# Performance work log

Hardware: AMD Instinct MI355X
Metric: run time of the kernel (lower is better)

The kernel has to match this reference:

```python
import jax, jax.numpy as jnp
import numpy as np

B, N, F_IN, F_HID, F_EMB, H, L_DIM = 8, 1024, 128, 128, 128, 8, 2


def _xavier(key, shape, fan_in, fan_out):
    lim = np.sqrt(6.0 / (fan_in + fan_out))
    return jax.random.uniform(key, shape, jnp.float32, -lim, lim)


def setup_inputs() -> dict:
    key = jax.random.key(0)
    ks = jax.random.split(key, 16)
    x = jax.random.normal(ks[0], (B, N, F_IN), jnp.float32)
    # sparse 0/1 adjacency with self loops (avoids fully-masked softmax rows)
    adj = (jax.random.uniform(ks[1], (B, N, N)) < 0.05).astype(jnp.float32)
    adj = jnp.maximum(adj, jnp.eye(N, dtype=jnp.float32)[None])
    def gat_params(k, f_in, f_out):
        k1, k2, k3 = jax.random.split(k, 3)
        return (_xavier(k1, (H, f_in, f_out), f_in, f_out),
                _xavier(k2, (H, f_out, 1), f_out, 1),
                _xavier(k3, (H, f_out, 1), f_out, 1),
                jnp.zeros((f_out,), jnp.float32))
    w1, as1, ad1, b1 = gat_params(ks[2], F_IN, F_HID)
    w2, as2, ad2, b2 = gat_params(ks[3], F_HID, F_HID)
    w3, as3, ad3, b3 = gat_params(ks[4], F_HID, F_EMB)
    pred_in = F_HID * 2 + F_EMB  # hidden*(num_layers-1)+embedding, concat=True
    pw = _xavier(ks[5], (pred_in, L_DIM), pred_in, L_DIM)
    pb = jnp.zeros((L_DIM,), jnp.float32)
    return {"x": x, "adj": adj,
            "w1": w1, "as1": as1, "ad1": ad1, "b1": b1,
            "w2": w2, "as2": as2, "ad2": ad2, "b2": b2,
            "w3": w3, "as3": as3, "ad3": ad3, "b3": b3,
            "pw": pw, "pb": pb}


def gat_layer(h, adj, w, a_src, a_dst, bias):
    # h: [B,N,f_in] -> h_prime: [B,H,N,f_out]
    hp = jnp.einsum('bnf,hfo->bhno', h, w)
    t = jnp.tanh(hp)
    s = jnp.einsum('bhno,hoi->bhni', t, a_src)[..., 0]  # [B,H,N]
    d = jnp.einsum('bhno,hoi->bhni', t, a_dst)[..., 0]  # [B,H,N]
    scores = s[:, :, :, None] + d[:, :, None, :]        # [B,H,N,N]
    scores = jnp.where(scores >= 0, scores, 0.2 * scores)  # LeakyReLU(0.2)
    scores = jnp.where(adj[:, None, :, :] > 0, scores, -jnp.inf)
    attn = jax.nn.softmax(scores, axis=-1)  # dropout disabled (eval mode)
    out = jnp.einsum('bhnm,bhmo->bhno', attn, hp) + bias
    return out.mean(axis=1)  # merge heads -> [B,N,f_out]


def reference(x, adj, w1, as1, ad1, b1, w2, as2, ad2, b2, w3, as3, ad3, b3, pw, pb):
    x1 = jax.nn.relu(gat_layer(x, adj, w1, as1, ad1, b1))
    x2 = jax.nn.relu(gat_layer(x1, adj, w2, as2, ad2, b2))
    x3 = gat_layer(x2, adj, w3, as3, ad3, b3)
    x_all = jnp.concatenate([x1, x2, x3], axis=2)  # [B,N,pred_in]
    pooled = jnp.max(x_all, axis=1)                # max over nodes -> [B,pred_in]
    return pooled @ pw + pb                        # [B,label_dim]
```

## Files before the change

kernel.cpp:

```cpp
#include <hip/hip_runtime.h>
#include <hip/hip_fp16.h>

#define BB 8
#define NN 1024
#define FF 128
#define HH 8

typedef _Float16 f16;
typedef f16  f16x8 __attribute__((ext_vector_type(8)));
typedef f16  f16x4 __attribute__((ext_vector_type(4)));
typedef float f32x4 __attribute__((ext_vector_type(4)));

#define L2E 1.44269504f

__global__ void k_pre(const float* __restrict__ x, f16* __restrict__ x16a,
                      const float* __restrict__ w1, const float* __restrict__ w2,
                      const float* __restrict__ w3, f16* __restrict__ wB,
                      const float* __restrict__ adj, unsigned* __restrict__ am){
  int bid = blockIdx.x, t = threadIdx.x;
  if (bid < 512){
    int i = (bid*256 + t)*8;
    float4 a = *(const float4*)(x+i), b = *(const float4*)(x+i+4);
    f16x8 v;
    v[0]=(f16)a.x; v[1]=(f16)a.y; v[2]=(f16)a.z; v[3]=(f16)a.w;
    v[4]=(f16)b.x; v[5]=(f16)b.y; v[6]=(f16)b.z; v[7]=(f16)b.w;
    *(f16x8*)(x16a+i) = v;
  } else if (bid < 704){
    int e = (bid-512)*256 + t;
    int fc = e & 15, c = (e>>4)&127, h = (e>>11)&7, l = e>>14;
    const float* w = (l==0) ? w1 : ((l==1) ? w2 : w3);
    f16x8 v;
    #pragma unroll
    for(int j=0;j<8;j++) v[j] = (f16)w[(h*128 + fc*8 + j)*128 + c];
    *(f16x8*)(wB + (((l*8+h)*16 + fc)*128 + c)*8) = v;
  } else {
    int wv = t >> 6, lane = t & 63;
    int r = (bid-704)*4 + wv;
    const float* row = adj + (long)r*1024;
    for(int g=0; g<16; g++){
      float v = row[g*64 + lane];
      unsigned long long mb = __ballot(v > 0.0f);
      if (lane == 0){
        am[r*32 + 2*g]   = (unsigned)mb;
        am[r*32 + 2*g+1] = (unsigned)(mb >> 32);
      }
    }
  }
}

__global__ __launch_bounds__(256,2) void k_hp(
    const f16* __restrict__ xin,
    const f16* __restrict__ wBl,
    const float* __restrict__ asrc, const float* __restrict__ adst,
    f16* __restrict__ hpB,
    float* __restrict__ sarr, float* __restrict__ darr)
{
  __shared__ f16 xs[128*136];
  __shared__ float asl[128], adl[128];
  int t = threadIdx.x;
  int bid = blockIdx.x;
  int it = bid & 7, h = (bid>>3)&7, b = bid>>6;
  int i0 = it*128;
  {
    const f16* src = xin + (long)(b*1024 + i0)*128;
    int fc = t & 15, r0 = t >> 4;
    #pragma unroll
    for(int p=0;p<8;p++){
      int r = r0 + p*16;
      f16x8 v = *(const f16x8*)(src + r*128 + fc*8);
      *(f16x8*)(xs + r*136 + fc*8) = v;
    }
  }
  if (t < 128){ asl[t] = asrc[h*128+t]; adl[t] = adst[h*128+t]; }
  __syncthreads();

  int lane = t & 63, wv = t>>6, wr = wv>>1, wc = wv&1;
  int mq = lane & 15, quad = lane >> 4;
  f32x4 acc[4][4];
  #pragma unroll
  for(int a=0;a<4;a++)
    #pragma unroll
    for(int c=0;c<4;c++) acc[a][c] = (f32x4){0.f,0.f,0.f,0.f};

  const f16* wh = wBl + h*16*128*8;
  #pragma unroll
  for(int ks=0; ks<4; ks++){
    f16x8 af[4], bf[4];
    #pragma unroll
    for(int mt=0; mt<4; mt++)
      af[mt] = *(const f16x8*)(xs + (wr*64 + mt*16 + mq)*136 + ks*32 + quad*8);
    #pragma unroll
    for(int nt=0; nt<4; nt++){
      int c  = wc*64 + nt*16 + mq;
      int fc = ks*4 + quad;
      bf[nt] = *(const f16x8*)(wh + (fc*128 + c)*8);
    }
    #pragma unroll
    for(int mt=0; mt<4; mt++)
      #pragma unroll
      for(int nt=0; nt<4; nt++)
        acc[mt][nt] = __builtin_amdgcn_mfma_f32_16x16x32_f16(af[mt], bf[nt], acc[mt][nt], 0,0,0);
  }
  __syncthreads();
  f16* tt = xs;
  f16* hpb = hpB + (long)(b*8+h)*128*128*8;
  #pragma unroll
  for(int mt=0; mt<4; mt++){
    #pragma unroll
    for(int nt=0; nt<4; nt++){
      int c = wc*64 + nt*16 + mq;
      f16x4 pk;
      #pragma unroll
      for(int rg=0; rg<4; rg++){
        float v = acc[mt][nt][rg];
        pk[rg] = (f16)v;
        int il = wr*64 + mt*16 + quad*4 + rg;
        float e2 = __expf(2.0f*v);
        float th = 1.0f - 2.0f*__builtin_amdgcn_rcpf(e2 + 1.0f);
        tt[il*136 + c] = (f16)th;
      }
      int il0 = wr*64 + mt*16 + quad*4;
      int inode = i0 + il0;
      *(f16x4*)(hpb + ((long)(inode>>3)*128 + c)*8 + (inode&7)) = pk;
    }
  }
  __syncthreads();
  {
    int r = t>>1, hf = t&1;
    float s_p = 0.f, d_p = 0.f;
    #pragma unroll
    for(int q=0;q<8;q++){
      f16x8 tv = *(const f16x8*)(tt + r*136 + hf*64 + q*8);
      #pragma unroll
      for(int j=0;j<8;j++){
        float tvf = (float)tv[j];
        int c = hf*64 + q*8 + j;
        s_p = fmaf(tvf, asl[c], s_p);
        d_p = fmaf(tvf, adl[c], d_p);
      }
    }
    s_p += __shfl_xor(s_p, 1);
    d_p += __shfl_xor(d_p, 1);
    if (hf == 0){
      sarr[(b*8+h)*1024 + i0 + r] = s_p;
      darr[(b*8+h)*1024 + i0 + r] = d_p;
    }
  }
}

__global__ __launch_bounds__(256,4) void k_attn(
    const f16* __restrict__ hpB,
    const float* __restrict__ sarr, const float* __restrict__ darr,
    const unsigned* __restrict__ am,
    f16* __restrict__ part,
    float* __restrict__ zpart)
{
  __shared__ float ddl[512];
  __shared__ float wred[4];
  __shared__ f16 Pl[2][128*40];
  int t = threadIdx.x;
  int bid = blockIdx.x;
  int bh = bid & 63, q = bid >> 6;
  int jh = q & 1, it = q >> 1;
  int i0 = it*128, j0 = jh*512;
  int b = bh >> 3;

  {
    float4 v = *(const float4*)(darr + bh*1024 + t*4);
    float mx = fmaxf(fmaxf(v.x,v.y), fmaxf(v.z,v.w));
    #pragma unroll
    for(int o=1;o<64;o<<=1) mx = fmaxf(mx, __shfl_xor(mx, o));
    if ((t&63)==0) wred[t>>6] = mx;
    int base = t*4 - j0;
    if (base >= 0 && base < 512){
      float4 s = make_float4(v.x*L2E, v.y*L2E, v.z*L2E, v.w*L2E);
      *(float4*)(ddl + base) = s;
    }
  }
  __syncthreads();
  float Dml = fmaxf(fmaxf(wred[0],wred[1]), fmaxf(wred[2],wred[3])) * L2E;

  int prow = t>>1, pjg = t&1;
  float srowl = sarr[bh*1024 + i0 + prow] * L2E;
  float ml = srowl + Dml;
  float mrowl = fmaxf(ml, 0.2f*ml);
  const unsigned* amrow = am + ((long)(b*1024 + i0 + prow))*32 + jh*16;

  int lane = t&63, wv = t>>6, wr = wv>>1, wc = wv&1;
  int mq = lane&15, quad = lane>>4;
  const f16* hpb = hpB + (long)bh*128*128*8;
  f32x4 acc[4][4];
  #pragma unroll
  for(int a=0;a<4;a++)
    #pragma unroll
    for(int c=0;c<4;c++) acc[a][c] = (f32x4){0.f,0.f,0.f,0.f};
  float zacc = 0.f;
  f16x8 zerov = (f16x8){0,0,0,0,0,0,0,0};

  unsigned wcur = amrow[0];
  for(int jt=0; jt<16; jt++){
    f16x8 bf[4];
    #pragma unroll
    for(int nt=0;nt<4;nt++){
      int c  = wc*64 + nt*16 + mq;
      int jc = jh*64 + jt*4 + quad;
      bf[nt] = *(const f16x8*)(hpb + (jc*128 + c)*8);
    }
    unsigned wnx = (jt < 15) ? amrow[jt+1] : 0u;
    f16* Pb = Pl[jt&1];
    f16* myp = Pb + prow*40 + pjg*16;
    *(f16x8*)(myp)     = zerov;
    *(f16x8*)(myp + 8) = zerov;
    unsigned word = (wcur >> (pjg*16)) & 0xffffu;
    const float* dloc = ddl + jt*32 + pjg*16;
    while(word){
      int j = __builtin_ctz(word);
      word &= word - 1u;
      float xl  = srowl + dloc[j];
      float scl = fmaxf(xl, 0.2f*xl);
      float e   = __builtin_amdgcn_exp2f(scl - mrowl);
      zacc += e;
      myp[j] = (f16)e;
    }
    __syncthreads();
    #pragma unroll
    for(int mt=0;mt<4;mt++){
      f16x8 a = *(const f16x8*)(Pb + (wr*64 + mt*16 + mq)*40 + quad*8);
      #pragma unroll
      for(int nt=0;nt<4;nt++)
        acc[mt][nt] = __builtin_amdgcn_mfma_f32_16x16x32_f16(a, bf[nt], acc[mt][nt], 0,0,0);
    }
    wcur = wnx;
  }
  zacc += __shfl_xor(zacc, 1);
  if (pjg == 0) zpart[(jh*64 + bh)*1024 + i0 + prow] = zacc;
  f16* pout = part + ((long)(jh*64 + bh)*1024 + i0)*128;
  #pragma unroll
  for(int mt=0;mt<4;mt++){
    #pragma unroll
    for(int nt=0;nt<4;nt++){
      int c = wc*64 + nt*16 + mq;
      #pragma unroll
      for(int rg=0;rg<4;rg++){
        int il = wr*64 + mt*16 + quad*4 + rg;
        pout[il*128 + c] = (f16)acc[mt][nt][rg];
      }
    }
  }
}

__global__ void k_fin(const f16* __restrict__ part, const float* __restrict__ zp,
                      const float* __restrict__ bias,
                      f16* __restrict__ x16, float* __restrict__ pmax, int do_relu){
  __shared__ float pm[16][128];
  int t = threadIdx.x;
  int idx = blockIdx.x*256 + t;
  int c8 = idx & 15, n = (idx>>4)&1023, b = idx>>14;
  float s[8];
  #pragma unroll
  for(int j=0;j<8;j++) s[j] = 0.f;
  #pragma unroll
  for(int h=0;h<8;h++){
    int bh = b*8 + h;
    float zi = 0.125f / (zp[bh*1024 + n] + zp[65536 + bh*1024 + n]);
    f16x8 p0 = *(const f16x8*)(part + ((long)bh*1024 + n)*128 + c8*8);
    f16x8 p1 = *(const f16x8*)(part + ((long)(64+bh)*1024 + n)*128 + c8*8);
    #pragma unroll
    for(int j=0;j<8;j++) s[j] = fmaf((float)p0[j] + (float)p1[j], zi, s[j]);
  }
  f16x8 h8;
  float ov[8];
  #pragma unroll
  for(int j=0;j<8;j++){
    float v = s[j] + bias[c8*8 + j];
    if (do_relu) v = fmaxf(v, 0.f);
    ov[j] = v;
    h8[j] = (f16)v;
  }
  if (x16) *(f16x8*)(x16 + ((long)(b*1024+n))*128 + c8*8) = h8;
  #pragma unroll
  for(int j=0;j<8;j++) pm[n&15][c8*8+j] = ov[j];
  __syncthreads();
  if (t < 128){
    float m = pm[0][t];
    #pragma unroll
    for(int r=1;r<16;r++) m = fmaxf(m, pm[r][t]);
    pmax[blockIdx.x*128 + t] = m;
  }
}

__global__ void k_pool2(const float* __restrict__ pmax, const float* __restrict__ pw,
                        const float* __restrict__ pb, float* __restrict__ out){
  __shared__ float pl[384];
  int b = blockIdx.x, t = threadIdx.x;
  for(int f = t; f < 384; f += 256){
    int l = f >> 7, c = f & 127;
    const float* p = pmax + l*65536 + b*64*128 + c;
    float mx = -3.4e38f;
    #pragma unroll 8
    for(int k=0;k<64;k++) mx = fmaxf(mx, p[k*128]);
    pl[f] = mx;
  }
  __syncthreads();
  if (t < 64){
    float a0 = 0.f, a1 = 0.f;
    #pragma unroll
    for(int k=0;k<6;k++){
      int f = t + 64*k;
      float v = pl[f];
      a0 = fmaf(v, pw[f*2],   a0);
      a1 = fmaf(v, pw[f*2+1], a1);
    }
    #pragma unroll
    for(int o=1;o<64;o<<=1){ a0 += __shfl_xor(a0,o); a1 += __shfl_xor(a1,o); }
    if (t == 0){ out[b*2] = a0 + pb[0]; out[b*2+1] = a1 + pb[1]; }
  }
}

extern "C" void kernel_launch(void* const* d_in, const int* in_sizes, int n_in,
                              void* d_out, int out_size, void* d_ws, size_t ws_size,
                              hipStream_t stream) {
  const float* x   = (const float*)d_in[0];
  const float* adj = (const float*)d_in[1];
  const float* w1  = (const float*)d_in[2];
  const float* as1 = (const float*)d_in[3];
  const float* ad1 = (const float*)d_in[4];
  const float* b1  = (const float*)d_in[5];
  const float* w2  = (const float*)d_in[6];
  const float* as2 = (const float*)d_in[7];
  const float* ad2 = (const float*)d_in[8];
  const float* b2  = (const float*)d_in[9];
  const float* w3  = (const float*)d_in[10];
  const float* as3 = (const float*)d_in[11];
  const float* ad3 = (const float*)d_in[12];
  const float* b3  = (const float*)d_in[13];
  const float* pw  = (const float*)d_in[14];
  const float* pb  = (const float*)d_in[15];

  char* ws = (char*)d_ws;
  f16*      x16a = (f16*)ws;                 ws += (size_t)1048576*2;
  f16*      x16b = (f16*)ws;                 ws += (size_t)1048576*2;
  f16*      wB   = (f16*)ws;                 ws += (size_t)393216*2;
  unsigned* am   = (unsigned*)ws;            ws += (size_t)8*1024*32*4;
  f16*      hpB  = (f16*)ws;                 ws += (size_t)8*8*1024*128*2;
  float*    sarr = (float*)ws;               ws += (size_t)65536*4;
  float*    darr = (float*)ws;               ws += (size_t)65536*4;
  f16*      part = (f16*)ws;                 ws += (size_t)2*64*1024*128*2;
  float*    zp   = (float*)ws;               ws += (size_t)2*65536*4;
  float*    pmax = (float*)ws;               ws += (size_t)3*512*128*4;

  k_pre<<<2752, 256, 0, stream>>>(x, x16a, w1, w2, w3, wB, adj, am);

  k_hp  <<<512, 256, 0, stream>>>(x16a, wB,            as1, ad1, hpB, sarr, darr);
  k_attn<<<1024,256, 0, stream>>>(hpB, sarr, darr, am, part, zp);
  k_fin <<<512, 256, 0, stream>>>(part, zp, b1, x16b, pmax,           1);
  k_hp  <<<512, 256, 0, stream>>>(x16b, wB + 131072,   as2, ad2, hpB, sarr, darr);
  k_attn<<<1024,256, 0, stream>>>(hpB, sarr, darr, am, part, zp);
  k_fin <<<512, 256, 0, stream>>>(part, zp, b2, x16a, pmax + 65536,   1);
  k_hp  <<<512, 256, 0, stream>>>(x16a, wB + 262144,   as3, ad3, hpB, sarr, darr);
  k_attn<<<1024,256, 0, stream>>>(hpB, sarr, darr, am, part, zp);
  k_fin <<<512, 256, 0, stream>>>(part, zp, b3, nullptr, pmax + 131072, 0);

  k_pool2<<<8, 256, 0, stream>>>(pmax, pw, pb, (float*)d_out);
}
```

Before: 256.8 us.

## Restructure GAT attention kernel: full-row tiles, software-pipelined P build, in-kernel normalization

The attention kernel now gives each block 64 rows over all 1024 columns instead of splitting the columns in halves. This removes the second partial output buffer and the separate row-sum array. The next column tile's P entries and B fragments are built and loaded while MFMAs run on the current tile, using a double-buffered shared P. Rows are normalized by the reciprocal of their sum inside the kernel, and the output is staged through LDS for coalesced vector stores, so the finishing kernel only sums the heads. The cost is a longer serial loop per block, fewer accumulators per wave, and four threads per row for mask expansion.

After: 260.1 us. No clear change (+1.3%).

```diff
diff --git a/kernel.cpp b/kernel.cpp
--- a/kernel.cpp
+++ b/kernel.cpp
@@ -152,105 +152,150 @@
     const f16* __restrict__ hpB,
     const float* __restrict__ sarr, const float* __restrict__ darr,
     const unsigned* __restrict__ am,
-    f16* __restrict__ part,
-    float* __restrict__ zpart)
+    f16* __restrict__ part)
 {
-  __shared__ float ddl[512];
+  __shared__ float ddl[1024];
   __shared__ float wred[4];
-  __shared__ f16 Pl[2][128*40];
+  __shared__ float zl[64];
+  __shared__ f16 Pl[2][64*72];
   int t = threadIdx.x;
   int bid = blockIdx.x;
-  int bh = bid & 63, q = bid >> 6;
-  int jh = q & 1, it = q >> 1;
-  int i0 = it*128, j0 = jh*512;
+  int bh = bid & 63, it = bid >> 6;
+  int i0 = it*64;
   int b = bh >> 3;
+
+  int lane = t&63, wv = t>>6;
+  int mq = lane&15, quad = lane>>4;
+  const f16* hpb = hpB + (long)bh*128*128*8;
 
   {
     float4 v = *(const float4*)(darr + bh*1024 + t*4);
     float mx = fmaxf(fmaxf(v.x,v.y), fmaxf(v.z,v.w));
     #pragma unroll
     for(int o=1;o<64;o<<=1) mx = fmaxf(mx, __shfl_xor(mx, o));
-    if ((t&63)==0) wred[t>>6] = mx;
-    int base = t*4 - j0;
-    if (base >= 0 && base < 512){
-      float4 s = make_float4(v.x*L2E, v.y*L2E, v.z*L2E, v.w*L2E);
-      *(float4*)(ddl + base) = s;
-    }
-  }
+    if (lane == 0) wred[wv] = mx;
+    *(float4*)(ddl + t*4) = make_float4(v.x*L2E, v.y*L2E, v.z*L2E, v.w*L2E);
+  }
+
+  int prow = t>>2, pg = t&3;
+  float srowl = sarr[bh*1024 + i0 + prow] * L2E;
+  const unsigned* amrow = am + ((long)(b*1024 + i0 + prow))*32;
+  int wsel = pg >> 1, wsh = (pg&1)*16;
+
+  f16x8 bcur[4], bnx[4];
+  #pragma unroll
+  for(int kk=0;kk<2;kk++)
+    #pragma unroll
+    for(int nt=0;nt<2;nt++){
+      int c  = wv*32 + nt*16 + mq;
+      int jc = kk*4 + quad;
+      bcur[kk*2+nt] = *(const f16x8*)(hpb + ((long)jc*128 + c)*8);
+    }
+  unsigned wcur = amrow[wsel];
+  unsigned wnx  = amrow[2 + wsel];
+
   __syncthreads();
   float Dml = fmaxf(fmaxf(wred[0],wred[1]), fmaxf(wred[2],wred[3])) * L2E;
-
-  int prow = t>>1, pjg = t&1;
-  float srowl = sarr[bh*1024 + i0 + prow] * L2E;
   float ml = srowl + Dml;
   float mrowl = fmaxf(ml, 0.2f*ml);
-  const unsigned* amrow = am + ((long)(b*1024 + i0 + prow))*32 + jh*16;
-
-  int lane = t&63, wv = t>>6, wr = wv>>1, wc = wv&1;
-  int mq = lane&15, quad = lane>>4;
-  const f16* hpb = hpB + (long)bh*128*128*8;
-  f32x4 acc[4][4];
-  #pragma unroll
-  for(int a=0;a<4;a++)
-    #pragma unroll
-    for(int c=0;c<4;c++) acc[a][c] = (f32x4){0.f,0.f,0.f,0.f};
+
+  f32x4 acc[4][2];
+  #pragma unroll
+  for(int a=0;a<4;a++){ acc[a][0] = (f32x4){0.f,0.f,0.f,0.f}; acc[a][1] = (f32x4){0.f,0.f,0.f,0.f}; }
   float zacc = 0.f;
   f16x8 zerov = (f16x8){0,0,0,0,0,0,0,0};
 
-  unsigned wcur = amrow[0];
-  for(int jt=0; jt<16; jt++){
-    f16x8 bf[4];
-    #pragma unroll
-    for(int nt=0;nt<4;nt++){
-      int c  = wc*64 + nt*16 + mq;
-      int jc = jh*64 + jt*4 + quad;
-      bf[nt] = *(const f16x8*)(hpb + (jc*128 + c)*8);
-    }
-    unsigned wnx = (jt < 15) ? amrow[jt+1] : 0u;
-    f16* Pb = Pl[jt&1];
-    f16* myp = Pb + prow*40 + pjg*16;
-    *(f16x8*)(myp)     = zerov;
-    *(f16x8*)(myp + 8) = zerov;
-    unsigned word = (wcur >> (pjg*16)) & 0xffffu;
-    const float* dloc = ddl + jt*32 + pjg*16;
+  {
+    f16* myp = Pl[0] + prow*72 + pg*16;
+    *(f16x8*)myp = zerov; *(f16x8*)(myp+8) = zerov;
+    unsigned word = (wcur >> wsh) & 0xffffu;
+    const float* dloc = ddl + pg*16;
     while(word){
-      int j = __builtin_ctz(word);
-      word &= word - 1u;
+      int j = __builtin_ctz(word); word &= word - 1u;
       float xl  = srowl + dloc[j];
       float scl = fmaxf(xl, 0.2f*xl);
       float e   = __builtin_amdgcn_exp2f(scl - mrowl);
       zacc += e;
       myp[j] = (f16)e;
     }
+  }
+  __syncthreads();
+
+  for(int jt=0; jt<16; jt++){
+    if (jt < 15){
+      #pragma unroll
+      for(int kk=0;kk<2;kk++)
+        #pragma unroll
+        for(int nt=0;nt<2;nt++){
+          int c  = wv*32 + nt*16 + mq;
+          int jc = (jt+1)*8 + kk*4 + quad;
+          bnx[kk*2+nt] = *(const f16x8*)(hpb + ((long)jc*128 + c)*8);
+        }
+      unsigned wfut = (jt < 14) ? amrow[(jt+2)*2 + wsel] : 0u;
+      f16* myp = Pl[(jt+1)&1] + prow*72 + pg*16;
+      *(f16x8*)myp = zerov; *(f16x8*)(myp+8) = zerov;
+      unsigned word = (wnx >> wsh) & 0xffffu;
+      const float* dloc = ddl + (jt+1)*64 + pg*16;
+      while(word){
+        int j = __builtin_ctz(word); word &= word - 1u;
+        float xl  = srowl + dloc[j];
+        float scl = fmaxf(xl, 0.2f*xl);
+        float e   = __builtin_amdgcn_exp2f(scl - mrowl);
+        zacc += e;
+        myp[j] = (f16)e;
+      }
+      wnx = wfut;
+    }
+    const f16* Pc = Pl[jt&1];
+    #pragma unroll
+    for(int kk=0;kk<2;kk++){
+      #pragma unroll
+      for(int mt=0;mt<4;mt++){
+        f16x8 a = *(const f16x8*)(Pc + (mt*16+mq)*72 + kk*32 + quad*8);
+        #pragma unroll
+        for(int nt=0;nt<2;nt++)
+          acc[mt][nt] = __builtin_amdgcn_mfma_f32_16x16x32_f16(a, bcur[kk*2+nt], acc[mt][nt], 0,0,0);
+      }
+    }
     __syncthreads();
-    #pragma unroll
-    for(int mt=0;mt<4;mt++){
-      f16x8 a = *(const f16x8*)(Pb + (wr*64 + mt*16 + mq)*40 + quad*8);
-      #pragma unroll
-      for(int nt=0;nt<4;nt++)
-        acc[mt][nt] = __builtin_amdgcn_mfma_f32_16x16x32_f16(a, bf[nt], acc[mt][nt], 0,0,0);
-    }
-    wcur = wnx;
-  }
+    if (jt < 15){
+      #pragma unroll
+      for(int q=0;q<4;q++) bcur[q] = bnx[q];
+    }
+  }
+
   zacc += __shfl_xor(zacc, 1);
-  if (pjg == 0) zpart[(jh*64 + bh)*1024 + i0 + prow] = zacc;
-  f16* pout = part + ((long)(jh*64 + bh)*1024 + i0)*128;
+  zacc += __shfl_xor(zacc, 2);
+  if (pg == 0) zl[prow] = zacc;
+  __syncthreads();
+
+  f16* Ps = (f16*)Pl;
   #pragma unroll
   for(int mt=0;mt<4;mt++){
     #pragma unroll
-    for(int nt=0;nt<4;nt++){
-      int c = wc*64 + nt*16 + mq;
-      #pragma unroll
-      for(int rg=0;rg<4;rg++){
-        int il = wr*64 + mt*16 + quad*4 + rg;
-        pout[il*128 + c] = (f16)acc[mt][nt][rg];
-      }
-    }
-  }
-}
-
-__global__ void k_fin(const f16* __restrict__ part, const float* __restrict__ zp,
-                      const float* __restrict__ bias,
+    for(int rg=0;rg<4;rg++){
+      int il = mt*16 + quad*4 + rg;
+      float zi = 0.125f * __builtin_amdgcn_rcpf(zl[il]);
+      #pragma unroll
+      for(int nt=0;nt<2;nt++){
+        int c = wv*32 + nt*16 + mq;
+        Ps[il*136 + c] = (f16)(acc[mt][nt][rg] * zi);
+      }
+    }
+  }
+  __syncthreads();
+  {
+    int r = t>>2, g = t&3;
+    f16* dst = part + ((long)bh*1024 + i0 + r)*128 + g*32;
+    const f16* srcp = Ps + r*136 + g*32;
+    *(f16x8*)(dst)    = *(const f16x8*)(srcp);
+    *(f16x8*)(dst+8)  = *(const f16x8*)(srcp+8);
+    *(f16x8*)(dst+16) = *(const f16x8*)(srcp+16);
+    *(f16x8*)(dst+24) = *(const f16x8*)(srcp+24);
+  }
+}
+
+__global__ void k_fin(const f16* __restrict__ part, const float* __restrict__ bias,
                       f16* __restrict__ x16, float* __restrict__ pmax, int do_relu){
   __shared__ float pm[16][128];
   int t = threadIdx.x;
@@ -262,11 +307,9 @@
   #pragma unroll
   for(int h=0;h<8;h++){
     int bh = b*8 + h;
-    float zi = 0.125f / (zp[bh*1024 + n] + zp[65536 + bh*1024 + n]);
     f16x8 p0 = *(const f16x8*)(part + ((long)bh*1024 + n)*128 + c8*8);
-    f16x8 p1 = *(const f16x8*)(part + ((long)(64+bh)*1024 + n)*128 + c8*8);
-    #pragma unroll
-    for(int j=0;j<8;j++) s[j] = fmaf((float)p0[j] + (float)p1[j], zi, s[j]);
+    #pragma unroll
+    for(int j=0;j<8;j++) s[j] += (float)p0[j];
   }
   f16x8 h8;
   float ov[8];
@@ -345,21 +388,20 @@
   f16*      hpB  = (f16*)ws;                 ws += (size_t)8*8*1024*128*2;
   float*    sarr = (float*)ws;               ws += (size_t)65536*4;
   float*    darr = (float*)ws;               ws += (size_t)65536*4;
-  f16*      part = (f16*)ws;                 ws += (size_t)2*64*1024*128*2;
-  float*    zp   = (float*)ws;               ws += (size_t)2*65536*4;
+  f16*      part = (f16*)ws;                 ws += (size_t)64*1024*128*2;
   float*    pmax = (float*)ws;               ws += (size_t)3*512*128*4;
 
   k_pre<<<2752, 256, 0, stream>>>(x, x16a, w1, w2, w3, wB, adj, am);
 
   k_hp  <<<512, 256, 0, stream>>>(x16a, wB,            as1, ad1, hpB, sarr, darr);
-  k_attn<<<1024,256, 0, stream>>>(hpB, sarr, darr, am, part, zp);
-  k_fin <<<512, 256, 0, stream>>>(part, zp, b1, x16b, pmax,           1);
+  k_attn<<<1024,256, 0, stream>>>(hpB, sarr, darr, am, part);
+  k_fin <<<512, 256, 0, stream>>>(part, b1, x16b, pmax,           1);
   k_hp  <<<512, 256, 0, stream>>>(x16b, wB + 131072,   as2, ad2, hpB, sarr, darr);
-  k_attn<<<1024,256, 0, stream>>>(hpB, sarr, darr, am, part, zp);
-  k_fin <<<512, 256, 0, stream>>>(part, zp, b2, x16a, pmax + 65536,   1);
+  k_attn<<<1024,256, 0, stream>>>(hpB, sarr, darr, am, part);
+  k_fin <<<512, 256, 0, stream>>>(part, b2, x16a, pmax + 65536,   1);
   k_hp  <<<512, 256, 0, stream>>>(x16a, wB + 262144,   as3, ad3, hpB, sarr, darr);
-  k_attn<<<1024,256, 0, stream>>>(hpB, sarr, darr, am, part, zp);
-  k_fin <<<512, 256, 0, stream>>>(part, zp, b3, nullptr, pmax + 131072, 0);
+  k_attn<<<1024,256, 0, stream>>>(hpB, sarr, darr, am, part);
+  k_fin <<<512, 256, 0, stream>>>(part, b3, nullptr, pmax + 131072, 0);
 
   k_pool2<<<8, 256, 0, stream>>>(pmax, pw, pb, (float*)d_out);
 }
```
